# Kernel tuning notes

Hardware: AMD Instinct MI355X
Metric: run time of the kernel (lower is better)

Reference implementation:

```python
import jax, jax.numpy as jnp
import numpy as np


def setup_inputs() -> dict:
    key = jax.random.key(0)
    ks = jax.random.split(key, 10)
    b, n, d = 4, 64, 64
    E = 4096
    node_emb = jax.random.normal(ks[0], (b * n, d), dtype=jnp.float32)
    path_emb = jax.random.normal(ks[1], (b, n, n, d), dtype=jnp.float32)
    edge_index = jax.random.randint(ks[2], (2, E), 0, b * n, dtype=jnp.int64)
    # learned params, stored as (in, out) so application is x @ W + b
    W_hz = jax.random.normal(ks[3], (d, d), dtype=jnp.float32) / np.sqrt(d)
    b_hz = jnp.zeros((d,), dtype=jnp.float32)
    W_zz = jax.random.normal(ks[4], (3 * d, d), dtype=jnp.float32) / np.sqrt(3 * d)
    b_zz = jnp.zeros((d,), dtype=jnp.float32)
    W_nm = jax.random.normal(ks[5], (2 * d, d), dtype=jnp.float32) / np.sqrt(2 * d)
    b_nm = jnp.zeros((d,), dtype=jnp.float32)
    return {
        "node_emb": node_emb, "path_emb": path_emb, "edge_index": edge_index,
        "W_hz": W_hz, "b_hz": b_hz, "W_zz": W_zz, "b_zz": b_zz,
        "W_nm": W_nm, "b_nm": b_nm,
    }


def reference(node_emb, path_emb, edge_index, W_hz, b_hz, W_zz, b_zz, W_nm, b_nm):
    b, n, _, d = path_emb.shape
    # ---- PathConv (aggr='max') ----
    z = path_emb @ W_hz + b_hz                                  # (b, n, n, d)
    # tropical (max-plus) matmul over paths: z_conv[b,i,j,d] = max_k z[b,i,k,d] + z[b,k,j,d]
    z_conv = jnp.max(z[:, :, :, None, :] + z[:, None, :, :, :], axis=2)  # (b, n, n, d)
    z = jnp.maximum(z_conv, z)                                  # path_aggr mode='max'
    ne = node_emb.reshape(b, n, d)
    n_i = jnp.broadcast_to(ne[:, :, None, :], (b, n, n, d))
    n_j = jnp.broadcast_to(ne[:, None, :, :], (b, n, n, d))
    u_path = jax.nn.relu(jnp.concatenate([n_i, z, n_j], axis=-1) @ W_zz + b_zz)
    # ---- MPLayer (default message = x_j, aggr='add'; edge_attr unused) ----
    src, dst = edge_index[0], edge_index[1]
    aggr_msg = jax.ops.segment_sum(node_emb[src], dst, num_segments=node_emb.shape[0])
    u_node = jax.nn.relu(jnp.concatenate([node_emb, aggr_msg], axis=-1) @ W_nm + b_nm)
    # residual
    return (u_node + node_emb, u_path + path_emb)
```

## Files before the change

kernel.cpp:

```cpp
#include <hip/hip_runtime.h>


__global__ __launch_bounds__(1024) void k_pathlin_node(
    const float* __restrict__ ne, const float* __restrict__ pe,
    const int* __restrict__ eidx,
    const float* __restrict__ Whz, const float* __restrict__ bhz,
    const float* __restrict__ Wzz,
    const float* __restrict__ Wnm, const float* __restrict__ bnm,
    float* __restrict__ zt, float* __restrict__ a1, float* __restrict__ a3,
    float* __restrict__ out0) {
  int bi = blockIdx.x;
  int b = bi >> 6, i = bi & 63;
  int t = threadIdx.x, lane = t & 63, w = t >> 6;
  __shared__ float sP[4096];
  __shared__ float sW[4096];
  __shared__ float part[16][64];
  __shared__ float nl[64], al[64];
  ((float4*)sP)[t] = ((const float4*)(pe + (size_t)bi * 4096))[t];
  ((float4*)sW)[t] = ((const float4*)Whz)[t];
  float bv = bhz[lane];
  if (w == 0) nl[lane] = ne[bi * 64 + lane];
  __syncthreads();
  float acc[4] = {bv, bv, bv, bv};
  int k0 = w * 4;
#pragma unroll
  for (int c = 0; c < 64; c += 4) {
    float w0 = sW[(c + 0) * 64 + lane], w1 = sW[(c + 1) * 64 + lane];
    float w2 = sW[(c + 2) * 64 + lane], w3 = sW[(c + 3) * 64 + lane];
#pragma unroll
    for (int kk = 0; kk < 4; ++kk) {
      const float4 p = *(const float4*)&sP[(k0 + kk) * 64 + c];
      acc[kk] += p.x * w0 + p.y * w1 + p.z * w2 + p.w * w3;
    }
  }
  float* dst = zt + (size_t)b * 262144 + (size_t)lane * 4096 + (size_t)i * 64 + k0;
  *(float4*)dst = make_float4(acc[0], acc[1], acc[2], acc[3]);
  __syncthreads();
  int* elist = (int*)sP;
  const int* srcv = eidx;
  const int* dstv = eidx + 4096;
  int cntw = 0;
  unsigned long long ltmask = (lane == 63) ? 0x7fffffffffffffffull
                                           : ((1ull << lane) - 1ull);
#pragma unroll
  for (int q = 0; q < 4; ++q) {
    int e2 = w * 256 + q * 64 + lane;
    bool match = (dstv[e2] == bi);
    unsigned long long mask = __ballot(match);
    if (match) {
      int pos = cntw + __popcll(mask & ltmask);
      elist[w * 256 + pos] = srcv[e2];
    }
    cntw += __popcll(mask);
  }
  float accA = 0.f;
  for (int m = 0; m < cntw; ++m) accA += ne[elist[w * 256 + m] * 64 + lane];
  part[w][lane] = accA;
  __syncthreads();
  if (w == 0) {
    float s = 0.f;
#pragma unroll
    for (int p2 = 0; p2 < 16; ++p2) s += part[p2][lane];
    al[lane] = s;
  } else if (w == 2) {
    const float* nr = ne + bi * 64;
    float s1 = 0.f;
    for (int d2 = 0; d2 < 64; ++d2) s1 += nr[d2] * Wzz[d2 * 64 + lane];
    a1[bi * 64 + lane] = s1;
  } else if (w == 3) {
    const float* nr = ne + bi * 64;
    float s3 = 0.f;
    for (int d2 = 0; d2 < 64; ++d2) s3 += nr[d2] * Wzz[(128 + d2) * 64 + lane];
    a3[bi * 64 + lane] = s3;
  }
  __syncthreads();
  {
    float s = 0.f;
#pragma unroll
    for (int dd = 0; dd < 4; ++dd) {
      int d2 = w * 4 + dd;
      s += nl[d2] * Wnm[d2 * 64 + lane] + al[d2] * Wnm[(64 + d2) * 64 + lane];
    }
    part[w][lane] = s;
  }
  __syncthreads();
  if (w == 0) {
    float v = bnm[lane];
#pragma unroll
    for (int p2 = 0; p2 < 16; ++p2) v += part[p2][lane];
    v = fmaxf(v, 0.f);
    out0[bi * 64 + lane] = v + nl[lane];
  }
}

__global__ __launch_bounds__(1024) void k_tropical(
    const float* __restrict__ zt, float* __restrict__ zt2) {
  int slice = blockIdx.x;
  int t = threadIdx.x, lane = t & 63, w = t >> 6;
  __shared__ float A[4096];
  const float* Ag = zt + (size_t)slice * 4096;
  ((float4*)A)[t] = ((const float4*)Ag)[t];
  __syncthreads();
  int i0 = w * 4;
  float acc[4];
#pragma unroll
  for (int ii = 0; ii < 4; ++ii) acc[ii] = A[(i0 + ii) * 64 + lane];
#pragma unroll
  for (int k = 0; k < 64; k += 4) {
    float c0 = A[(k + 0) * 64 + lane], c1 = A[(k + 1) * 64 + lane];
    float c2 = A[(k + 2) * 64 + lane], c3 = A[(k + 3) * 64 + lane];
#pragma unroll
    for (int ii = 0; ii < 4; ++ii) {
      const float4 a = *(const float4*)&A[(i0 + ii) * 64 + k];
      float m0 = fmaxf(a.x + c0, a.y + c1);
      float m1 = fmaxf(a.z + c2, a.w + c3);
      acc[ii] = fmaxf(acc[ii], fmaxf(m0, m1));
    }
  }
  float* Og = zt2 + (size_t)slice * 4096 + (size_t)i0 * 64;
#pragma unroll
  for (int ii = 0; ii < 4; ++ii) Og[ii * 64 + lane] = acc[ii];
}

__global__ __launch_bounds__(1024) void k_upath(
    const float* __restrict__ zt2, const float* __restrict__ Wzz,
    const float* __restrict__ bzz, const float* __restrict__ a1,
    const float* __restrict__ a3, const float* __restrict__ pe,
    float* __restrict__ out1) {
  int bi = blockIdx.x;
  int b = bi >> 6, i = bi & 63;
  int t = threadIdx.x, lane = t & 63, w = t >> 6;
  __shared__ float sZ[4096];
  __shared__ float sW2[4096];
  {
    int d2 = t >> 4, jo = (t & 15) * 4;
    const float* src = zt2 + (size_t)b * 262144 + (size_t)d2 * 4096
                     + (size_t)i * 64 + jo;
    *(float4*)&sZ[d2 * 64 + jo] = *(const float4*)src;
  }
  ((float4*)sW2)[t] = ((const float4*)(Wzz + 4096))[t];
  float base = a1[bi * 64 + lane] + bzz[lane];
  __syncthreads();
  int j0 = w * 4;
  float acc[4] = {base, base, base, base};
#pragma unroll
  for (int d = 0; d < 64; ++d) {
    const float4 z4 = *(const float4*)&sZ[d * 64 + j0];
    float wv = sW2[d * 64 + lane];
    acc[0] += z4.x * wv;
    acc[1] += z4.y * wv;
    acc[2] += z4.z * wv;
    acc[3] += z4.w * wv;
  }
  const float* a3b = a3 + (size_t)b * 4096;
  size_t ob = (size_t)bi * 4096 + (size_t)j0 * 64;
#pragma unroll
  for (int jj = 0; jj < 4; ++jj) {
    float v = acc[jj] + a3b[(j0 + jj) * 64 + lane];
    v = fmaxf(v, 0.f);
    out1[ob + jj * 64 + lane] = v + pe[ob + jj * 64 + lane];
  }
}

extern "C" void kernel_launch(void* const* d_in, const int* in_sizes, int n_in,
                              void* d_out, int out_size, void* d_ws, size_t ws_size,
                              hipStream_t stream) {
  const float* node = (const float*)d_in[0];
  const float* pe   = (const float*)d_in[1];
  const int*   eidx = (const int*)d_in[2];
  const float* Whz  = (const float*)d_in[3];
  const float* bhz  = (const float*)d_in[4];
  const float* Wzz  = (const float*)d_in[5];
  const float* bzz  = (const float*)d_in[6];
  const float* Wnm  = (const float*)d_in[7];
  const float* bnm  = (const float*)d_in[8];
  float* out0 = (float*)d_out;
  float* out1 = out0 + 16384;
  float* zt  = (float*)d_ws;
  float* zt2 = zt + 1048576;
  float* a1  = zt2 + 1048576;
  float* a3  = a1 + 16384;

  hipLaunchKernelGGL(k_pathlin_node, dim3(256), dim3(1024), 0, stream,
                     node, pe, eidx, Whz, bhz, Wzz, Wnm, bnm, zt, a1, a3, out0);
  hipLaunchKernelGGL(k_tropical, dim3(256), dim3(1024), 0, stream, zt, zt2);
  hipLaunchKernelGGL(k_upath, dim3(256), dim3(1024), 0, stream,
                     zt2, Wzz, bzz, a1, a3, pe, out1);
}
```

Before: 27.31 us.

## Hold per-lane operand columns in registers instead of shared memory across kernels

The path linear kernel now has each thread load its path row straight from global memory into registers and compute four output channels, so path_emb is no longer staged in shared memory and the transposed z writes change pattern. The tropical kernel preloads each lane's column into a 64-entry register array from global memory. The upath kernel keeps its Wzz slice in registers instead of shared memory. The goal is fewer LDS reads, but 64+ live floats per thread at 1024 threads per block push register pressure and can cause spills, and the z stores become strided.

New measurement: 32.06 us. 17.4% more time.

```diff
diff --git a/kernel.cpp b/kernel.cpp
--- a/kernel.cpp
+++ b/kernel.cpp
@@ -12,31 +12,33 @@
   int bi = blockIdx.x;
   int b = bi >> 6, i = bi & 63;
   int t = threadIdx.x, lane = t & 63, w = t >> 6;
-  __shared__ float sP[4096];
+  int d0 = w * 4;
   __shared__ float sW[4096];
+  __shared__ int elist[4096];
   __shared__ float part[16][64];
   __shared__ float nl[64], al[64];
-  ((float4*)sP)[t] = ((const float4*)(pe + (size_t)bi * 4096))[t];
   ((float4*)sW)[t] = ((const float4*)Whz)[t];
-  float bv = bhz[lane];
+  const float* peb = pe + (size_t)bi * 4096 + (size_t)lane * 64;
+  float4 pr[16];
+#pragma unroll
+  for (int c4 = 0; c4 < 16; ++c4) pr[c4] = *(const float4*)(peb + c4 * 4);
+  float acc[4] = {bhz[d0], bhz[d0 + 1], bhz[d0 + 2], bhz[d0 + 3]};
+  __syncthreads();
+#pragma unroll
+  for (int c = 0; c < 64; ++c) {
+    const float4 wv = *(const float4*)&sW[c * 64 + d0];
+    float pv = (c & 2) ? ((c & 1) ? pr[c >> 2].w : pr[c >> 2].z)
+                       : ((c & 1) ? pr[c >> 2].y : pr[c >> 2].x);
+    acc[0] += pv * wv.x;
+    acc[1] += pv * wv.y;
+    acc[2] += pv * wv.z;
+    acc[3] += pv * wv.w;
+  }
+  float* zb = zt + (size_t)b * 262144 + (size_t)i * 64 + lane;
+#pragma unroll
+  for (int dd = 0; dd < 4; ++dd) zb[(size_t)(d0 + dd) * 4096] = acc[dd];
+
   if (w == 0) nl[lane] = ne[bi * 64 + lane];
-  __syncthreads();
-  float acc[4] = {bv, bv, bv, bv};
-  int k0 = w * 4;
-#pragma unroll
-  for (int c = 0; c < 64; c += 4) {
-    float w0 = sW[(c + 0) * 64 + lane], w1 = sW[(c + 1) * 64 + lane];
-    float w2 = sW[(c + 2) * 64 + lane], w3 = sW[(c + 3) * 64 + lane];
-#pragma unroll
-    for (int kk = 0; kk < 4; ++kk) {
-      const float4 p = *(const float4*)&sP[(k0 + kk) * 64 + c];
-      acc[kk] += p.x * w0 + p.y * w1 + p.z * w2 + p.w * w3;
-    }
-  }
-  float* dst = zt + (size_t)b * 262144 + (size_t)lane * 4096 + (size_t)i * 64 + k0;
-  *(float4*)dst = make_float4(acc[0], acc[1], acc[2], acc[3]);
-  __syncthreads();
-  int* elist = (int*)sP;
   const int* srcv = eidx;
   const int* dstv = eidx + 4096;
   int cntw = 0;
@@ -100,20 +102,21 @@
   __shared__ float A[4096];
   const float* Ag = zt + (size_t)slice * 4096;
   ((float4*)A)[t] = ((const float4*)Ag)[t];
-  __syncthreads();
+  float colreg[64];
+#pragma unroll
+  for (int k = 0; k < 64; ++k) colreg[k] = Ag[k * 64 + lane];
   int i0 = w * 4;
   float acc[4];
 #pragma unroll
-  for (int ii = 0; ii < 4; ++ii) acc[ii] = A[(i0 + ii) * 64 + lane];
+  for (int ii = 0; ii < 4; ++ii) acc[ii] = Ag[(i0 + ii) * 64 + lane];
+  __syncthreads();
 #pragma unroll
   for (int k = 0; k < 64; k += 4) {
-    float c0 = A[(k + 0) * 64 + lane], c1 = A[(k + 1) * 64 + lane];
-    float c2 = A[(k + 2) * 64 + lane], c3 = A[(k + 3) * 64 + lane];
 #pragma unroll
     for (int ii = 0; ii < 4; ++ii) {
       const float4 a = *(const float4*)&A[(i0 + ii) * 64 + k];
-      float m0 = fmaxf(a.x + c0, a.y + c1);
-      float m1 = fmaxf(a.z + c2, a.w + c3);
+      float m0 = fmaxf(a.x + colreg[k], a.y + colreg[k + 1]);
+      float m1 = fmaxf(a.z + colreg[k + 2], a.w + colreg[k + 3]);
       acc[ii] = fmaxf(acc[ii], fmaxf(m0, m1));
     }
   }
@@ -131,14 +134,15 @@
   int b = bi >> 6, i = bi & 63;
   int t = threadIdx.x, lane = t & 63, w = t >> 6;
   __shared__ float sZ[4096];
-  __shared__ float sW2[4096];
   {
     int d2 = t >> 4, jo = (t & 15) * 4;
     const float* src = zt2 + (size_t)b * 262144 + (size_t)d2 * 4096
                      + (size_t)i * 64 + jo;
     *(float4*)&sZ[d2 * 64 + jo] = *(const float4*)src;
   }
-  ((float4*)sW2)[t] = ((const float4*)(Wzz + 4096))[t];
+  float wreg[64];
+#pragma unroll
+  for (int d = 0; d < 64; ++d) wreg[d] = Wzz[(64 + d) * 64 + lane];
   float base = a1[bi * 64 + lane] + bzz[lane];
   __syncthreads();
   int j0 = w * 4;
@@ -146,7 +150,7 @@
 #pragma unroll
   for (int d = 0; d < 64; ++d) {
     const float4 z4 = *(const float4*)&sZ[d * 64 + j0];
-    float wv = sW2[d * 64 + lane];
+    float wv = wreg[d];
     acc[0] += z4.x * wv;
     acc[1] += z4.y * wv;
     acc[2] += z4.z * wv;
```
